# Optimization experiments

Measured on AMD Instinct MI355X. Metric: run time of the kernel, lower is better.

## Reference

```python
import jax, jax.numpy as jnp
import numpy as np

FACTOR = 2  # upsample factor per spatial dim


def setup_inputs() -> dict:
    key = jax.random.key(0)
    k1, k2, k3 = jax.random.split(key, 3)
    B, C_in, C_out, H, W_ = 8, 128, 128, 64, 64
    x = jax.random.normal(k1, (B, C_in, H, W_), dtype=jnp.float32)
    # conv3x3 params (OIHW), fan-in scaled init like torch Conv2d default scale
    fan_in = C_in * 3 * 3
    W = jax.random.normal(k2, (C_out, C_in, 3, 3), dtype=jnp.float32) / np.sqrt(fan_in)
    b = jax.random.normal(k3, (C_out,), dtype=jnp.float32) * 0.01
    return {"x": x, "W": W, "b": b}


def reference(x, W, b):
    h = jnp.repeat(jnp.repeat(x, FACTOR, axis=2), FACTOR, axis=3)  # [B,C,2H,2W]
    # conv3x3: stride 1, padding 1
    out = jax.lax.conv_general_dilated(
        h, W,
        window_strides=(1, 1),
        padding=((1, 1), (1, 1)),
        dimension_numbers=("NCHW", "OIHW", "NCHW"),
    )
    return out + b[None, :, None, None]
```

## Files before the change

kernel.cpp:

```cpp
#include <hip/hip_runtime.h>
#include <stdint.h>

typedef short bf16x8 __attribute__((ext_vector_type(8)));
typedef float f32x4 __attribute__((ext_vector_type(4)));

#define NCI 128
#define NCO 128
#define HIN 64
#define NB  8

__device__ __forceinline__ unsigned short f32_to_bf16(float f) {
    union { float f; uint32_t u; } v; v.f = f;
    return (unsigned short)((v.u + 0x7FFFu + ((v.u >> 16) & 1u)) >> 16);
}

__device__ __forceinline__ float weff_sum(const float* wp, int py, int px, int ty, int tx) {
    float s = 0.f;
    #pragma unroll
    for (int ky = 0; ky < 3; ++ky) {
        bool iy = (py == 0) ? (ty == 0 ? (ky == 0) : (ky >= 1))
                            : (ty == 0 ? (ky <= 1) : (ky == 2));
        if (!iy) continue;
        #pragma unroll
        for (int kx = 0; kx < 3; ++kx) {
            bool ix = (px == 0) ? (tx == 0 ? (kx == 0) : (kx >= 1))
                                : (tx == 0 ? (kx <= 1) : (kx == 2));
            if (ix) s += wp[ky * 3 + kx];
        }
    }
    return s;
}

__global__ __launch_bounds__(256) void weff6_kernel(
        const float* __restrict__ W, unsigned short* __restrict__ Aw6) {
    int idx = blockIdx.x * 256 + threadIdx.x;
    int e   = idx & 7;
    int rl  = (idx >> 3) & 15;
    int pl  = (idx >> 7) & 3;
    int f   = (idx >> 9) & 1;
    int cob = (idx >> 10) & 3;
    int kt  = (idx >> 12) & 15;
    int par = idx >> 16;
    int co = cob * 32 + f * 16 + rl;
    int k  = kt * 32 + pl * 8 + e;
    int tap = k >> 7, ci = k & 127;
    Aw6[idx] = f32_to_bf16(weff_sum(W + (co * NCI + ci) * 9,
                                    par >> 1, par & 1, tap >> 1, tap & 1));
}

__global__ __launch_bounds__(512, 4) void upconv14_kernel(
        const float* __restrict__ x, const unsigned short* __restrict__ Aw6,
        const float* __restrict__ bv, float* __restrict__ out) {
    __shared__ __align__(16) unsigned short smem[16896];
    const int d = blockIdx.x;
    const int bi = d & 7;
    const int py = (d >> 3) & 1;
    const int oy0 = d >> 4;
    const int tid = threadIdx.x, lane = tid & 63, wv = tid >> 6;
    const int pxw = wv & 1, cob = wv >> 1;
    const int rl = lane & 15, pl = lane >> 4;
    const int par = py * 2 + pxw;

    if (tid < 64) {
        int r = tid >> 5, cz = ((tid >> 4) & 1) * 65, q = tid & 15;
        *(bf16x8*)&smem[((r * 66 + cz) * 16 + q) * 8] = (bf16x8){0,0,0,0,0,0,0,0};
    }
    #pragma unroll
    for (int i = 0; i < 4; ++i) {
        const int tk = wv * 4 + i;
        const int r = tk >> 4, oct = tk & 15;
        const int grow = oy0 + py - 1 + r;
        const bool ok = (unsigned)grow < 64u;
        const float* xp = x + ((size_t)(bi * NCI + oct * 8) * HIN + (ok ? grow : 0)) * HIN + lane;
        bf16x8 v;
        #pragma unroll
        for (int j = 0; j < 8; ++j) {
            float f = ok ? xp[(size_t)j * (HIN * HIN)] : 0.f;
            v[j] = (short)f32_to_bf16(f);
        }
        const int c = lane + 1;
        *(bf16x8*)&smem[((r * 66 + c) * 16 + (oct ^ (c & 15))) * 8] = v;
    }
    __syncthreads();

    f32x4 acc[2][4];
    #pragma unroll
    for (int i = 0; i < 2; ++i)
        #pragma unroll
        for (int j = 0; j < 4; ++j)
            acc[i][j] = (f32x4){0.f, 0.f, 0.f, 0.f};

    bf16x8 Abuf[3][2];
    auto loadA = [&](bf16x8* Ad, int kt) {
        const unsigned short* p = Aw6 + (((par * 64) + kt * 4 + cob) << 10) + lane * 8;
        Ad[0] = *(const bf16x8*)p;
        Ad[1] = *(const bf16x8*)(p + 512);
    };
    loadA(Abuf[0], 0);
    loadA(Abuf[1], 1);
    loadA(Abuf[2], 2);

    const int c0 = rl + pxw;
    #pragma unroll
    for (int kp = 0; kp < 16; ++kp) {
        bf16x8* Ac = Abuf[kp % 3];
        const int ty = kp >> 3, tx = (kp >> 2) & 1, cq = kp & 3;
        __builtin_amdgcn_s_setprio(1);
        #pragma unroll
        for (int f = 0; f < 4; ++f) {
            const int c = c0 + f * 16 + tx;
            const int q = (cq * 4 + pl) ^ (c & 15);
            bf16x8 bfr = *(const bf16x8*)&smem[((ty * 66 + c) * 16 + q) * 8];
            #pragma unroll
            for (int fm = 0; fm < 2; ++fm)
                acc[fm][f] = __builtin_amdgcn_mfma_f32_16x16x32_bf16(
                    Ac[fm], bfr, acc[fm][f], 0, 0, 0);
        }
        __builtin_amdgcn_s_setprio(0);
        if (kp + 3 < 16) loadA(Abuf[kp % 3], kp + 3);
    }
    __syncthreads();

    float* lf = (float*)smem;
    const int co_rd = tid >> 3;
    const int x16 = (tid & 7) * 16;
    const int yy = 2 * oy0 + py;
    #pragma unroll
    for (int b = 0; b < 2; ++b) {
        if ((cob >> 1) == b) {
            #pragma unroll
            for (int fm = 0; fm < 2; ++fm)
                #pragma unroll
                for (int fn = 0; fn < 4; ++fn) {
                    const int xx = 2 * (fn * 16 + rl) + pxw;
                    #pragma unroll
                    for (int j = 0; j < 4; ++j) {
                        const int co_l = (cob & 1) * 32 + fm * 16 + pl * 4 + j;
                        lf[co_l * 132 + xx] = acc[fm][fn][j];
                    }
                }
        }
        asm volatile("s_waitcnt lgkmcnt(0)" ::: "memory");
        __builtin_amdgcn_s_barrier();
        const int co_g = b * 64 + co_rd;
        const float bb = bv[co_g];
        float* op = out + (((size_t)(bi * NCO + co_g)) << 14) + yy * 128 + x16;
        const float* sp = lf + co_rd * 132 + x16;
        #pragma unroll
        for (int qq = 0; qq < 4; ++qq) {
            f32x4 v = *(const f32x4*)(sp + qq * 4);
            v[0] += bb; v[1] += bb; v[2] += bb; v[3] += bb;
            *(f32x4*)(op + qq * 4) = v;
        }
        if (b == 0) __builtin_amdgcn_s_barrier();
    }
}

__global__ void weff_flat_kernel(const float* __restrict__ W,
                                 unsigned short* __restrict__ Aw) {
    int idx = blockIdx.x * 256 + threadIdx.x;
    int par = idx >> 16;
    int co  = (idx >> 9) & 127;
    int k   = idx & 511;
    int tap = k >> 7, ci = k & 127;
    Aw[idx] = f32_to_bf16(weff_sum(W + (co * NCI + ci) * 9,
                                   par >> 1, par & 1, tap >> 1, tap & 1));
}

__global__ __launch_bounds__(256) void upconv_fb_kernel(
        const float* __restrict__ x, const unsigned short* __restrict__ Aw,
        const float* __restrict__ bv, float* __restrict__ out) {
    __shared__ __align__(16) unsigned short A_lds[128 * 32];
    __shared__ __align__(16) unsigned short B_lds[128 * 32];
    const int par = blockIdx.y, py = par >> 1, px = par & 1;
    const int s0 = blockIdx.x * 128;
    const int bimg = s0 >> 12;
    const int oy0 = (s0 >> 6) & 63;
    const int tid = threadIdx.x;
    const int lane = tid & 63, wave = tid >> 6;
    const int wm = wave >> 1, wn = wave & 1;
    const float* xb = x + bimg * (NCI * HIN * HIN);
    f32x4 acc[4][4];
    #pragma unroll
    for (int i = 0; i < 4; ++i)
        #pragma unroll
        for (int j = 0; j < 4; ++j)
            acc[i][j] = (f32x4){0.f, 0.f, 0.f, 0.f};
    for (int kt = 0; kt < 16; ++kt) {
        const int tap = kt >> 2, ci0 = (kt & 3) * 32;
        const int ty = tap >> 1, tx = tap & 1;
        #pragma unroll
        for (int i = 0; i < 2; ++i) {
            int c = i * 256 + tid;
            *(bf16x8*)(&A_lds[c * 8]) = *(const bf16x8*)(Aw +
                ((par * 128 + (c >> 2)) * 512 + kt * 32 + (c & 3) * 8));
        }
        #pragma unroll
        for (int i = 0; i < 2; ++i) {
            int tsk = i * 256 + tid;
            int n = tsk & 127, kg = tsk >> 7;
            int r = n >> 6, ox = n & 63;
            int row = oy0 + r - 1 + py + ty;
            int col = ox - 1 + px + tx;
            bool ok = (row >= 0) & (row < HIN) & (col >= 0) & (col < HIN);
            const float* xp = xb + (((ci0 + kg * 8) * HIN + row) * HIN + col);
            bf16x8 v;
            #pragma unroll
            for (int q = 0; q < 8; ++q) {
                float f = ok ? xp[q * (HIN * HIN)] : 0.f;
                v[q] = (short)f32_to_bf16(f);
            }
            *(bf16x8*)(&B_lds[n * 32 + kg * 8]) = v;
        }
        __syncthreads();
        const int seg = (lane >> 4) * 8, rl2 = lane & 15;
        bf16x8 af[4], bfr[4];
        #pragma unroll
        for (int f = 0; f < 4; ++f)
            af[f] = *(const bf16x8*)(&A_lds[(wm * 64 + f * 16 + rl2) * 32 + seg]);
        #pragma unroll
        for (int f = 0; f < 4; ++f)
            bfr[f] = *(const bf16x8*)(&B_lds[(wn * 64 + f * 16 + rl2) * 32 + seg]);
        #pragma unroll
        for (int fm = 0; fm < 4; ++fm)
            #pragma unroll
            for (int fn = 0; fn < 4; ++fn)
                acc[fm][fn] = __builtin_amdgcn_mfma_f32_16x16x32_bf16(
                    af[fm], bfr[fn], acc[fm][fn], 0, 0, 0);
        __syncthreads();
    }
    #pragma unroll
    for (int fm = 0; fm < 4; ++fm) {
        const int co_b = wm * 64 + fm * 16 + (lane >> 4) * 4;
        float bias4[4];
        #pragma unroll
        for (int j = 0; j < 4; ++j) bias4[j] = bv[co_b + j];
        #pragma unroll
        for (int fn = 0; fn < 4; ++fn) {
            int n = wn * 64 + fn * 16 + (lane & 15);
            int s = s0 + n;
            int ox = s & 63, oy = (s >> 6) & 63, bi2 = s >> 12;
            int yy = 2 * oy + py, xx = 2 * ox + px;
            float* op = out + ((size_t)bi2 * 128 * 128 * 128) + (size_t)yy * 128 + xx;
            #pragma unroll
            for (int j = 0; j < 4; ++j)
                op[(size_t)(co_b + j) * (128 * 128)] = acc[fm][fn][j] + bias4[j];
        }
    }
}

extern "C" void kernel_launch(void* const* d_in, const int* in_sizes, int n_in,
                              void* d_out, int out_size, void* d_ws, size_t ws_size,
                              hipStream_t stream) {
    const float* x  = (const float*)d_in[0];
    const float* W  = (const float*)d_in[1];
    const float* bv = (const float*)d_in[2];
    float* out = (float*)d_out;
    unsigned short* Aw = (unsigned short*)d_ws;
    const size_t aw_bytes = (size_t)4 * 16 * 4 * 1024 * sizeof(unsigned short);

    if (ws_size >= aw_bytes) {
        weff6_kernel<<<1024, 256, 0, stream>>>(W, Aw);
        upconv14_kernel<<<1024, 512, 0, stream>>>(x, Aw, bv, out);
    } else {
        weff_flat_kernel<<<1024, 256, 0, stream>>>(W, Aw);
        upconv_fb_kernel<<<dim3(256, 4), 256, 0, stream>>>(x, Aw, bv, out);
    }
}
```

Measured before the change: 48.08 us.

## Switch main conv kernel to 32x32x16 MFMA tiles with 4-wave blocks

Result: faster. 47.00 us (-2.2%).

```diff
diff --git a/kernel.cpp b/kernel.cpp
--- a/kernel.cpp
+++ b/kernel.cpp
@@ -3,6 +3,7 @@
 
 typedef short bf16x8 __attribute__((ext_vector_type(8)));
 typedef float f32x4 __attribute__((ext_vector_type(4)));
+typedef float f32x16 __attribute__((ext_vector_type(16)));
 
 #define NCI 128
 #define NCO 128
@@ -31,25 +32,24 @@
     return s;
 }
 
-__global__ __launch_bounds__(256) void weff6_kernel(
-        const float* __restrict__ W, unsigned short* __restrict__ Aw6) {
+__global__ __launch_bounds__(256) void weff7_kernel(
+        const float* __restrict__ W, unsigned short* __restrict__ Aw7) {
     int idx = blockIdx.x * 256 + threadIdx.x;
     int e   = idx & 7;
-    int rl  = (idx >> 3) & 15;
-    int pl  = (idx >> 7) & 3;
-    int f   = (idx >> 9) & 1;
-    int cob = (idx >> 10) & 3;
-    int kt  = (idx >> 12) & 15;
+    int ln  = (idx >> 3) & 63;
+    int fm  = (idx >> 9) & 1;
+    int cob = (idx >> 10) & 1;
+    int s   = (idx >> 11) & 31;
     int par = idx >> 16;
-    int co = cob * 32 + f * 16 + rl;
-    int k  = kt * 32 + pl * 8 + e;
+    int co = cob * 64 + fm * 32 + (ln & 31);
+    int k  = s * 16 + (ln >> 5) * 8 + e;
     int tap = k >> 7, ci = k & 127;
-    Aw6[idx] = f32_to_bf16(weff_sum(W + (co * NCI + ci) * 9,
+    Aw7[idx] = f32_to_bf16(weff_sum(W + (co * NCI + ci) * 9,
                                     par >> 1, par & 1, tap >> 1, tap & 1));
 }
 
-__global__ __launch_bounds__(512, 4) void upconv14_kernel(
-        const float* __restrict__ x, const unsigned short* __restrict__ Aw6,
+__global__ __launch_bounds__(256, 4) void upconv15_kernel(
+        const float* __restrict__ x, const unsigned short* __restrict__ Aw7,
         const float* __restrict__ bv, float* __restrict__ out) {
     __shared__ __align__(16) unsigned short smem[16896];
     const int d = blockIdx.x;
@@ -58,16 +58,16 @@
     const int oy0 = d >> 4;
     const int tid = threadIdx.x, lane = tid & 63, wv = tid >> 6;
     const int pxw = wv & 1, cob = wv >> 1;
-    const int rl = lane & 15, pl = lane >> 4;
+    const int l31 = lane & 31, lh = lane >> 5;
     const int par = py * 2 + pxw;
 
     if (tid < 64) {
         int r = tid >> 5, cz = ((tid >> 4) & 1) * 65, q = tid & 15;
-        *(bf16x8*)&smem[((r * 66 + cz) * 16 + q) * 8] = (bf16x8){0,0,0,0,0,0,0,0};
-    }
-    #pragma unroll
-    for (int i = 0; i < 4; ++i) {
-        const int tk = wv * 4 + i;
+        *(bf16x8*)&smem[(((r * 66 + cz) << 4) + q) * 8] = (bf16x8){0,0,0,0,0,0,0,0};
+    }
+    #pragma unroll
+    for (int i = 0; i < 8; ++i) {
+        const int tk = wv * 8 + i;
         const int r = tk >> 4, oct = tk & 15;
         const int grow = oy0 + py - 1 + r;
         const bool ok = (unsigned)grow < 64u;
@@ -79,20 +79,22 @@
             v[j] = (short)f32_to_bf16(f);
         }
         const int c = lane + 1;
-        *(bf16x8*)&smem[((r * 66 + c) * 16 + (oct ^ (c & 15))) * 8] = v;
+        *(bf16x8*)&smem[(((r * 66 + c) << 4) + (oct ^ (c & 15))) * 8] = v;
     }
     __syncthreads();
 
-    f32x4 acc[2][4];
+    f32x16 acc[2][2];
     #pragma unroll
     for (int i = 0; i < 2; ++i)
         #pragma unroll
-        for (int j = 0; j < 4; ++j)
-            acc[i][j] = (f32x4){0.f, 0.f, 0.f, 0.f};
+        for (int j = 0; j < 2; ++j)
+            #pragma unroll
+            for (int q = 0; q < 16; ++q)
+                acc[i][j][q] = 0.f;
 
     bf16x8 Abuf[3][2];
-    auto loadA = [&](bf16x8* Ad, int kt) {
-        const unsigned short* p = Aw6 + (((par * 64) + kt * 4 + cob) << 10) + lane * 8;
+    auto loadA = [&](bf16x8* Ad, int s) {
+        const unsigned short* p = Aw7 + (((par * 32 + s) * 2 + cob) << 10) + lane * 8;
         Ad[0] = *(const bf16x8*)p;
         Ad[1] = *(const bf16x8*)(p + 512);
     };
@@ -100,59 +102,57 @@
     loadA(Abuf[1], 1);
     loadA(Abuf[2], 2);
 
-    const int c0 = rl + pxw;
-    #pragma unroll
-    for (int kp = 0; kp < 16; ++kp) {
-        bf16x8* Ac = Abuf[kp % 3];
-        const int ty = kp >> 3, tx = (kp >> 2) & 1, cq = kp & 3;
+    #pragma unroll
+    for (int s = 0; s < 32; ++s) {
+        bf16x8* Ac = Abuf[s % 3];
+        const int ty = s >> 4, tx = (s >> 3) & 1, qb = (s & 7) * 2;
         __builtin_amdgcn_s_setprio(1);
         #pragma unroll
-        for (int f = 0; f < 4; ++f) {
-            const int c = c0 + f * 16 + tx;
-            const int q = (cq * 4 + pl) ^ (c & 15);
-            bf16x8 bfr = *(const bf16x8*)&smem[((ty * 66 + c) * 16 + q) * 8];
+        for (int fn = 0; fn < 2; ++fn) {
+            const int c = l31 + fn * 32 + pxw + tx;
+            const int q = (qb + lh) ^ (c & 15);
+            bf16x8 bfr = *(const bf16x8*)&smem[(((ty * 66 + c) << 4) + q) * 8];
             #pragma unroll
             for (int fm = 0; fm < 2; ++fm)
-                acc[fm][f] = __builtin_amdgcn_mfma_f32_16x16x32_bf16(
-                    Ac[fm], bfr, acc[fm][f], 0, 0, 0);
+                acc[fm][fn] = __builtin_amdgcn_mfma_f32_32x32x16_bf16(
+                    Ac[fm], bfr, acc[fm][fn], 0, 0, 0);
         }
         __builtin_amdgcn_s_setprio(0);
-        if (kp + 3 < 16) loadA(Abuf[kp % 3], kp + 3);
+        if (s + 3 < 32) loadA(Abuf[s % 3], s + 3);
     }
     __syncthreads();
 
     float* lf = (float*)smem;
-    const int co_rd = tid >> 3;
-    const int x16 = (tid & 7) * 16;
+    const int co_rd = tid >> 2;
+    const int x32 = (tid & 3) * 32;
     const int yy = 2 * oy0 + py;
     #pragma unroll
     for (int b = 0; b < 2; ++b) {
-        if ((cob >> 1) == b) {
+        if (cob == b) {
             #pragma unroll
             for (int fm = 0; fm < 2; ++fm)
                 #pragma unroll
-                for (int fn = 0; fn < 4; ++fn) {
-                    const int xx = 2 * (fn * 16 + rl) + pxw;
+                for (int fn = 0; fn < 2; ++fn)
                     #pragma unroll
-                    for (int j = 0; j < 4; ++j) {
-                        const int co_l = (cob & 1) * 32 + fm * 16 + pl * 4 + j;
+                    for (int j = 0; j < 16; ++j) {
+                        const int row = (j & 3) + 8 * (j >> 2) + 4 * lh;
+                        const int co_l = fm * 32 + row;
+                        const int xx = 2 * (fn * 32 + l31) + pxw;
                         lf[co_l * 132 + xx] = acc[fm][fn][j];
                     }
-                }
-        }
-        asm volatile("s_waitcnt lgkmcnt(0)" ::: "memory");
-        __builtin_amdgcn_s_barrier();
+        }
+        __syncthreads();
         const int co_g = b * 64 + co_rd;
         const float bb = bv[co_g];
-        float* op = out + (((size_t)(bi * NCO + co_g)) << 14) + yy * 128 + x16;
-        const float* sp = lf + co_rd * 132 + x16;
-        #pragma unroll
-        for (int qq = 0; qq < 4; ++qq) {
+        float* op = out + (((size_t)(bi * NCO + co_g)) << 14) + yy * 128 + x32;
+        const float* sp = lf + co_rd * 132 + x32;
+        #pragma unroll
+        for (int qq = 0; qq < 8; ++qq) {
             f32x4 v = *(const f32x4*)(sp + qq * 4);
             v[0] += bb; v[1] += bb; v[2] += bb; v[3] += bb;
             *(f32x4*)(op + qq * 4) = v;
         }
-        if (b == 0) __builtin_amdgcn_s_barrier();
+        if (b == 0) __syncthreads();
     }
 }
 
@@ -257,11 +257,11 @@
     const float* bv = (const float*)d_in[2];
     float* out = (float*)d_out;
     unsigned short* Aw = (unsigned short*)d_ws;
-    const size_t aw_bytes = (size_t)4 * 16 * 4 * 1024 * sizeof(unsigned short);
+    const size_t aw_bytes = (size_t)4 * 32 * 2 * 2 * 512 * sizeof(unsigned short);
 
     if (ws_size >= aw_bytes) {
-        weff6_kernel<<<1024, 256, 0, stream>>>(W, Aw);
-        upconv14_kernel<<<1024, 512, 0, stream>>>(x, Aw, bv, out);
+        weff7_kernel<<<1024, 256, 0, stream>>>(W, Aw);
+        upconv15_kernel<<<1024, 256, 0, stream>>>(x, Aw, bv, out);
     } else {
         weff_flat_kernel<<<1024, 256, 0, stream>>>(W, Aw);
         upconv_fb_kernel<<<dim3(256, 4), 256, 0, stream>>>(x, Aw, bv, out);
```
